# Kernel optimization log

Measured on AMD Instinct MI355X. Metric: run time of the kernel, lower is better.

## Reference

```python
import jax, jax.numpy as jnp
import numpy as np

D_MODEL = 1024
N_HEADS = 16
HEAD_DIM = D_MODEL // N_HEADS
B, S = 2, 2048


def setup_inputs() -> dict:
    key = jax.random.key(0)
    ks = jax.random.split(key, 10)
    lin = lambda k: jax.random.normal(k, (D_MODEL, D_MODEL), jnp.float32) / np.sqrt(D_MODEL)
    return {
        "x": jax.random.normal(ks[0], (B, S, D_MODEL), jnp.float32),
        "W_boundary": lin(ks[1]),
        "b_boundary": jax.random.normal(ks[2], (D_MODEL,), jnp.float32) * 0.02,
        "W_q": lin(ks[3]),
        "b_q": jax.random.normal(ks[4], (D_MODEL,), jnp.float32) * 0.02,
        "W_k": lin(ks[5]),
        "b_k": jax.random.normal(ks[6], (D_MODEL,), jnp.float32) * 0.02,
        "W_v": lin(ks[7]),
        "b_v": jax.random.normal(ks[8], (D_MODEL,), jnp.float32) * 0.02,
        "radial_weights": jax.random.normal(ks[9], (N_HEADS, 1, 1), jnp.float32),
        "tropical_scale": jnp.ones((1,), jnp.float32),
    }


def tropical_softmax(x, scale):
    # max-plus algebra softmax: subtract max, rescale, normalize with eps
    x = (x - jnp.max(x, axis=-1, keepdims=True)) * scale
    e = jnp.exp(x)
    return e / (jnp.sum(e, axis=-1, keepdims=True) + 1e-8)


def reference(x, W_boundary, b_boundary, W_q, b_q, W_k, b_k, W_v, b_v,
              radial_weights, tropical_scale):
    bsz, seq, _ = x.shape
    boundary = x @ W_boundary.T + b_boundary  # [B,S,D]

    def heads(W, b):  # [B,S,D] -> [B,H,S,hd]
        return (x @ W.T + b).reshape(bsz, seq, N_HEADS, HEAD_DIM).transpose(0, 2, 1, 3)

    q = heads(W_q, b_q)
    k = heads(W_k, b_k)
    v = heads(W_v, b_v)

    q = q * jax.nn.sigmoid(radial_weights)  # broadcast [H,1,1]

    scores = jnp.einsum("bhqd,bhkd->bhqk", q, k) / np.sqrt(HEAD_DIM).astype(np.float32)
    attn = tropical_softmax(scores, tropical_scale)  # [B,H,S,S]

    out = jnp.einsum("bhqk,bhkd->bhqd", attn, v)
    out = out.transpose(0, 2, 1, 3).reshape(bsz, seq, D_MODEL)
    out = out + boundary
    return (out, attn)
```

## Files before the change

### kernel.cpp

```cpp
#include <hip/hip_runtime.h>

#define DM 1024
#define NH 16
#define HD 64
#define BB 2
#define SS 2048
#define MTOT (BB*SS)
#define NTOT (4*DM)

typedef __attribute__((ext_vector_type(8))) short short8;
typedef __attribute__((ext_vector_type(4))) float f32x4;

#define MFMA(a,b,c) __builtin_amdgcn_mfma_f32_16x16x32_bf16((a),(b),(c),0,0,0)

__device__ inline unsigned short f2bf(float f) {
  union { float f; unsigned u; } v; v.f = f;
  unsigned r = v.u + 0x7FFFu + ((v.u >> 16) & 1u);
  return (unsigned short)(r >> 16);
}

__device__ inline void gload_lds16(const void* g, void* l) {
  void* gnc = const_cast<void*>(g);
  __builtin_amdgcn_global_load_lds(
      (__attribute__((address_space(1))) void*)gnc,
      (__attribute__((address_space(3))) void*)l, 16, 0, 0);
}

__global__ __launch_bounds__(256) void k_convert(
    const float* __restrict__ x, const float* __restrict__ w0,
    const float* __restrict__ w1, const float* __restrict__ w2,
    const float* __restrict__ w3,
    unsigned short* __restrict__ xb, unsigned short* __restrict__ wb) {
  const int T4 = (MTOT * DM) / 4;
  int stride = gridDim.x * blockDim.x;
  for (int i = blockIdx.x * blockDim.x + threadIdx.x; i < 2 * T4; i += stride) {
    const float* src; unsigned short* dst;
    if (i < T4) { src = x + (size_t)i * 4; dst = xb + (size_t)i * 4; }
    else {
      int flat = (i - T4) * 4;
      int sel = flat >> 20;
      int off = flat & ((1 << 20) - 1);
      const float* w = (sel == 0) ? w0 : (sel == 1) ? w1 : (sel == 2) ? w2 : w3;
      src = w + off; dst = wb + flat;
    }
    float4 v = *(const float4*)src;
    ushort4 o; o.x = f2bf(v.x); o.y = f2bf(v.y); o.z = f2bf(v.z); o.w = f2bf(v.w);
    *(ushort4*)dst = o;
  }
}

__global__ __launch_bounds__(256) void k_proj(
    const unsigned short* __restrict__ xb, const unsigned short* __restrict__ wb,
    const float* __restrict__ bbd, const float* __restrict__ bq,
    const float* __restrict__ bk, const float* __restrict__ bv,
    const float* __restrict__ radial,
    float* __restrict__ outbd,
    unsigned short* __restrict__ qb, unsigned short* __restrict__ kb,
    unsigned short* __restrict__ vb) {
  __shared__ unsigned short lsA[128 * 64];
  __shared__ unsigned short lsB[128 * 64];
  const int tid = threadIdx.x;
  const int wave = tid >> 6, lane = tid & 63;
  const int wr = wave >> 1, wc = wave & 1;
  const int lin = blockIdx.y * gridDim.x + blockIdx.x;
  const int swz = (lin & 7) * 128 + (lin >> 3);
  const int m0 = (swz >> 5) * 128, n0 = (swz & 31) * 128;
  const int ro = lane & 15, gg = lane >> 4;
  const int srow = lane >> 3;
  const int scol = (lane & 7) * 8;
  f32x4 acc[4][4] = {};
  for (int kt = 0; kt < DM / 64; ++kt) {
    __syncthreads();
    #pragma unroll
    for (int i = 0; i < 4; ++i) {
      int c = wave * 4 + i;
      const unsigned short* ga = xb + (size_t)(m0 + c * 8 + srow) * DM + kt * 64 + scol;
      gload_lds16(ga, (void*)(lsA + c * 512));
      const unsigned short* gb = wb + (size_t)(n0 + c * 8 + srow) * DM + kt * 64 + scol;
      gload_lds16(gb, (void*)(lsB + c * 512));
    }
    __syncthreads();
    #pragma unroll
    for (int ks = 0; ks < 2; ++ks) {
      short8 a[4], b[4];
      int ko = ks * 32 + gg * 8;
      #pragma unroll
      for (int r = 0; r < 4; ++r)
        a[r] = *(const short8*)&lsA[(wr * 64 + r * 16 + ro) * 64 + ko];
      #pragma unroll
      for (int c = 0; c < 4; ++c)
        b[c] = *(const short8*)&lsB[(wc * 64 + c * 16 + ro) * 64 + ko];
      #pragma unroll
      for (int r = 0; r < 4; ++r)
        #pragma unroll
        for (int c = 0; c < 4; ++c)
          acc[r][c] = MFMA(a[r], b[c], acc[r][c]);
    }
  }
  const int which = n0 >> 10;
  #pragma unroll
  for (int r = 0; r < 4; ++r) {
    const int mbase = m0 + wr * 64 + r * 16 + gg * 4;
    #pragma unroll
    for (int c = 0; c < 4; ++c) {
      const int n = n0 + wc * 64 + c * 16 + ro;
      const int nn = n & 1023;
      #pragma unroll
      for (int j = 0; j < 4; ++j) {
        const int m = mbase + j;
        float v = acc[r][c][j];
        if (which == 0) {
          outbd[(size_t)m * DM + nn] = v + bbd[nn];
        } else {
          const int h = nn >> 6, d = nn & 63;
          const int b2 = m >> 11, s = m & 2047;
          const size_t o = (((size_t)(b2 * NH + h)) * SS + s) * HD + d;
          if (which == 1) {
            float sg = 1.f / (1.f + __expf(-radial[h]));
            qb[o] = f2bf((v + bq[nn]) * sg);
          } else if (which == 2) {
            kb[o] = f2bf(v + bk[nn]);
          } else {
            vb[o] = f2bf(v + bv[nn]);
          }
        }
      }
    }
  }
}

__global__ __launch_bounds__(256) void k_vt(
    const unsigned short* __restrict__ vb, unsigned short* __restrict__ vt) {
  __shared__ unsigned short t[64][65];
  const int bh = blockIdx.y, st = blockIdx.x;
  const int tid = threadIdx.x;
  const int r = tid >> 2, c4 = (tid & 3) * 16;
  const unsigned short* src = vb + ((size_t)bh * SS + st * 64 + r) * HD + c4;
  #pragma unroll
  for (int i = 0; i < 16; i += 4) {
    ushort4 v = *(const ushort4*)(src + i);
    t[r][c4 + i + 0] = v.x; t[r][c4 + i + 1] = v.y;
    t[r][c4 + i + 2] = v.z; t[r][c4 + i + 3] = v.w;
  }
  __syncthreads();
  const int dd = tid >> 2, s4 = (tid & 3) * 16;
  unsigned short* dst = vt + ((size_t)bh * HD + dd) * SS + st * 64 + s4;
  #pragma unroll
  for (int i = 0; i < 16; i += 4) {
    ushort4 o;
    o.x = t[s4 + i + 0][dd]; o.y = t[s4 + i + 1][dd];
    o.z = t[s4 + i + 2][dd]; o.w = t[s4 + i + 3][dd];
    *(ushort4*)(dst + i) = o;
  }
}

__global__ __launch_bounds__(256) void k_attn_pv(
    const unsigned short* __restrict__ qb, const unsigned short* __restrict__ kb,
    const unsigned short* __restrict__ vt, const float* __restrict__ tsc,
    float* __restrict__ attn, float* __restrict__ out) {
  __shared__ unsigned short lk[2][64 * 64];
  __shared__ unsigned short lv[2][64 * 64];
  __shared__ __align__(16) unsigned short pt[4][16 * 64];
  const int bh = blockIdx.y, qt = blockIdx.x;
  const int tid = threadIdx.x, wave = tid >> 6, lane = tid & 63;
  const int ro = lane & 15, gg = lane >> 4;

  const unsigned short* kb_bh = kb + (size_t)bh * SS * HD;
  const unsigned short* vt_bh = vt + (size_t)bh * HD * SS;

  int sr0, sc0, sr1, sc1;
  {
    int s0 = (wave * 2 + 0) * 64 + lane;
    int s1 = (wave * 2 + 1) * 64 + lane;
    sr0 = s0 >> 3; sc0 = (s0 & 7) ^ (sr0 & 7);
    sr1 = s1 >> 3; sc1 = (s1 & 7) ^ (sr1 & 7);
  }

#define STAGE_K(buf, kt) do { \
    const unsigned short* g = kb_bh + (size_t)(kt) * 64 * HD; \
    gload_lds16(g + sr0 * 64 + sc0 * 8, (void*)(lk[buf] + (wave * 2 + 0) * 512)); \
    gload_lds16(g + sr1 * 64 + sc1 * 8, (void*)(lk[buf] + (wave * 2 + 1) * 512)); \
  } while (0)
#define STAGE_V(buf, kt) do { \
    const unsigned short* g = vt_bh + (size_t)(kt) * 64; \
    gload_lds16(g + (size_t)sr0 * SS + sc0 * 8, (void*)(lv[buf] + (wave * 2 + 0) * 512)); \
    gload_lds16(g + (size_t)sr1 * SS + sc1 * 8, (void*)(lv[buf] + (wave * 2 + 1) * 512)); \
  } while (0)

  STAGE_K(0, 0);

  const unsigned short* qrow =
      qb + ((size_t)bh * SS + qt * 64 + wave * 16 + ro) * HD;
  short8 aq0 = *(const short8*)(qrow + gg * 8);
  short8 aq1 = *(const short8*)(qrow + 32 + gg * 8);
  const float fac = tsc[0] * 0.125f;

  __syncthreads();

  float psum = 0.f;
  int cur = 0;
  for (int ct = 0; ct < 32; ++ct) {
    if (ct < 31) STAGE_K(cur ^ 1, ct + 1);
    const unsigned short* kbuf = lk[cur];
    #pragma unroll
    for (int sub = 0; sub < 4; ++sub) {
      const int rr = sub * 16 + ro;
      const unsigned short* kr = kbuf + rr * 64;
      short8 b0 = *(const short8*)&kr[(gg ^ (rr & 7)) * 8];
      short8 b1 = *(const short8*)&kr[((4 + gg) ^ (rr & 7)) * 8];
      f32x4 sf = {};
      sf = MFMA(b0, aq0, sf);
      sf = MFMA(b1, aq1, sf);
      psum += __expf(sf[0] * fac) + __expf(sf[1] * fac)
            + __expf(sf[2] * fac) + __expf(sf[3] * fac);
    }
    __syncthreads();
    cur ^= 1;
  }
  STAGE_K(0, 0);
  STAGE_V(0, 0);
  psum += __shfl_xor(psum, 16);
  psum += __shfl_xor(psum, 32);
  const float rsum = 1.f / (psum + 1e-8f);
  __syncthreads();

  float* ab = attn + ((size_t)bh * SS + qt * 64 + wave * 16 + ro) * SS;
  unsigned short* pw = &pt[wave][0];
  f32x4 acc[4] = {};
  cur = 0;
  for (int ct = 0; ct < 32; ++ct) {
    asm volatile("s_waitcnt vmcnt(4)" ::: "memory");
    __builtin_amdgcn_s_barrier();
    if (ct < 31) { STAGE_K(cur ^ 1, ct + 1); STAGE_V(cur ^ 1, ct + 1); }
    const unsigned short* kbuf = lk[cur];
    const unsigned short* vbuf = lv[cur];
    #pragma unroll
    for (int sub = 0; sub < 4; ++sub) {
      const int rr = sub * 16 + ro;
      const unsigned short* kr = kbuf + rr * 64;
      short8 b0 = *(const short8*)&kr[(gg ^ (rr & 7)) * 8];
      short8 b1 = *(const short8*)&kr[((4 + gg) ^ (rr & 7)) * 8];
      f32x4 sf = {};
      sf = MFMA(b0, aq0, sf);
      sf = MFMA(b1, aq1, sf);
      f32x4 st;
      st[0] = __expf(sf[0] * fac) * rsum; st[1] = __expf(sf[1] * fac) * rsum;
      st[2] = __expf(sf[2] * fac) * rsum; st[3] = __expf(sf[3] * fac) * rsum;
      __builtin_nontemporal_store(st, (f32x4*)(ab + (ct * 4 + sub) * 16 + gg * 4));
      unsigned w0, w1;
      asm("v_cvt_pk_bf16_f32 %0, %1, %2" : "=v"(w0) : "v"(st[0]), "v"(st[1]));
      asm("v_cvt_pk_bf16_f32 %0, %1, %2" : "=v"(w1) : "v"(st[2]), "v"(st[3]));
      const int slot = (sub * 2 + (gg >> 1)) ^ (ro & 7);
      *(uint2*)((char*)pw + ro * 128 + slot * 16 + (gg & 1) * 8) = make_uint2(w0, w1);
    }
    #pragma unroll
    for (int ks = 0; ks < 2; ++ks) {
      const int pslot = (ks * 4 + gg) ^ (ro & 7);
      short8 pa = *(const short8*)((const char*)pw + ro * 128 + pslot * 16);
      #pragma unroll
      for (int dc = 0; dc < 4; ++dc) {
        const int rr = dc * 16 + ro;
        const int cc = (ks * 4 + gg) ^ (rr & 7);
        short8 bvf = *(const short8*)&vbuf[rr * 64 + cc * 8];
        acc[dc] = MFMA(pa, bvf, acc[dc]);
      }
    }
    cur ^= 1;
  }

  const int b2 = bh >> 4, h = bh & 15;
  const int s0 = qt * 64 + wave * 16 + gg * 4;
  #pragma unroll
  for (int dc = 0; dc < 4; ++dc)
    #pragma unroll
    for (int j = 0; j < 4; ++j) {
      size_t o = ((size_t)b2 * SS + s0 + j) * DM + h * HD + dc * 16 + ro;
      out[o] += acc[dc][j];
    }
#undef STAGE_K
#undef STAGE_V
}

extern "C" void kernel_launch(void* const* d_in, const int* in_sizes, int n_in,
                              void* d_out, int out_size, void* d_ws, size_t ws_size,
                              hipStream_t stream) {
  (void)in_sizes; (void)n_in; (void)out_size; (void)ws_size;
  const float* x   = (const float*)d_in[0];
  const float* Wb  = (const float*)d_in[1];
  const float* bb  = (const float*)d_in[2];
  const float* Wq  = (const float*)d_in[3];
  const float* bq  = (const float*)d_in[4];
  const float* Wk  = (const float*)d_in[5];
  const float* bk  = (const float*)d_in[6];
  const float* Wv  = (const float*)d_in[7];
  const float* bv  = (const float*)d_in[8];
  const float* rad = (const float*)d_in[9];
  const float* tsc = (const float*)d_in[10];

  float* out  = (float*)d_out;
  float* attn = out + (size_t)MTOT * DM;

  unsigned short* qb = (unsigned short*)d_ws;
  unsigned short* kb = qb + (size_t)4 * 1024 * 1024;
  unsigned short* vt = kb + (size_t)4 * 1024 * 1024;

  unsigned short* xb = (unsigned short*)attn;
  unsigned short* wb = xb + (size_t)4 * 1024 * 1024;
  unsigned short* vb = wb + (size_t)4 * 1024 * 1024;

  k_convert<<<2048, 256, 0, stream>>>(x, Wb, Wq, Wk, Wv, xb, wb);
  k_proj<<<dim3(32, 32), 256, 0, stream>>>(xb, wb, bb, bq, bk, bv, rad, out, qb, kb, vb);
  k_vt<<<dim3(32, 32), 256, 0, stream>>>(vb, vt);
  k_attn_pv<<<dim3(32, 32), 256, 0, stream>>>(qb, kb, vt, tsc, attn, out);
}
```

Baseline: 276.8 us.

## Deepen K prefetch to 4-stage ring in pass 1 and swizzle block order

Pass 1 of the attention kernel now uses a 4-buffer LDS ring with three K tiles in flight, replacing the double buffer and full __syncthreads with vmcnt waits plus barriers. The LDS is unified into one array that pass 2 reuses as K/V double buffers. The block index is also remapped so consecutive blocks spread across heads, which is meant to improve L2 locality or XCD distribution. The aim is to hide global-load latency in the score-recompute pass, at the cost of tighter manual waitcnt bookkeeping.

```diff
diff --git a/kernel.cpp b/kernel.cpp
--- a/kernel.cpp
+++ b/kernel.cpp
@@ -158,10 +158,11 @@
     const unsigned short* __restrict__ qb, const unsigned short* __restrict__ kb,
     const unsigned short* __restrict__ vt, const float* __restrict__ tsc,
     float* __restrict__ attn, float* __restrict__ out) {
-  __shared__ unsigned short lk[2][64 * 64];
-  __shared__ unsigned short lv[2][64 * 64];
+  __shared__ unsigned short lds[4][64 * 64];
   __shared__ __align__(16) unsigned short pt[4][16 * 64];
-  const int bh = blockIdx.y, qt = blockIdx.x;
+  const int p = blockIdx.y * gridDim.x + blockIdx.x;
+  const int t = (p & 7) * 128 + (p >> 3);
+  const int bh = t >> 5, qt = t & 31;
   const int tid = threadIdx.x, wave = tid >> 6, lane = tid & 63;
   const int ro = lane & 15, gg = lane >> 4;
 
@@ -178,16 +179,14 @@
 
 #define STAGE_K(buf, kt) do { \
     const unsigned short* g = kb_bh + (size_t)(kt) * 64 * HD; \
-    gload_lds16(g + sr0 * 64 + sc0 * 8, (void*)(lk[buf] + (wave * 2 + 0) * 512)); \
-    gload_lds16(g + sr1 * 64 + sc1 * 8, (void*)(lk[buf] + (wave * 2 + 1) * 512)); \
+    gload_lds16(g + sr0 * 64 + sc0 * 8, (void*)(lds[buf] + (wave * 2 + 0) * 512)); \
+    gload_lds16(g + sr1 * 64 + sc1 * 8, (void*)(lds[buf] + (wave * 2 + 1) * 512)); \
   } while (0)
 #define STAGE_V(buf, kt) do { \
     const unsigned short* g = vt_bh + (size_t)(kt) * 64; \
-    gload_lds16(g + (size_t)sr0 * SS + sc0 * 8, (void*)(lv[buf] + (wave * 2 + 0) * 512)); \
-    gload_lds16(g + (size_t)sr1 * SS + sc1 * 8, (void*)(lv[buf] + (wave * 2 + 1) * 512)); \
+    gload_lds16(g + (size_t)sr0 * SS + sc0 * 8, (void*)(lds[buf] + (wave * 2 + 0) * 512)); \
+    gload_lds16(g + (size_t)sr1 * SS + sc1 * 8, (void*)(lds[buf] + (wave * 2 + 1) * 512)); \
   } while (0)
-
-  STAGE_K(0, 0);
 
   const unsigned short* qrow =
       qb + ((size_t)bh * SS + qt * 64 + wave * 16 + ro) * HD;
@@ -195,13 +194,11 @@
   short8 aq1 = *(const short8*)(qrow + 32 + gg * 8);
   const float fac = tsc[0] * 0.125f;
 
-  __syncthreads();
+  STAGE_K(0, 0); STAGE_K(1, 1); STAGE_K(2, 2);
 
   float psum = 0.f;
-  int cur = 0;
-  for (int ct = 0; ct < 32; ++ct) {
-    if (ct < 31) STAGE_K(cur ^ 1, ct + 1);
-    const unsigned short* kbuf = lk[cur];
+  auto p1body = [&](int ct) {
+    const unsigned short* kbuf = lds[ct & 3];
     #pragma unroll
     for (int sub = 0; sub < 4; ++sub) {
       const int rr = sub * 16 + ro;
@@ -214,26 +211,40 @@
       psum += __expf(sf[0] * fac) + __expf(sf[1] * fac)
             + __expf(sf[2] * fac) + __expf(sf[3] * fac);
     }
-    __syncthreads();
-    cur ^= 1;
-  }
+  };
+  for (int ct = 0; ct < 30; ++ct) {
+    asm volatile("s_waitcnt vmcnt(4)" ::: "memory");
+    __builtin_amdgcn_s_barrier();
+    if (ct < 29) STAGE_K((ct + 3) & 3, ct + 3);
+    p1body(ct);
+  }
+  asm volatile("s_waitcnt vmcnt(2)" ::: "memory");
+  __builtin_amdgcn_s_barrier();
+  p1body(30);
+  asm volatile("s_waitcnt vmcnt(0)" ::: "memory");
+  __builtin_amdgcn_s_barrier();
+  p1body(31);
+
   STAGE_K(0, 0);
-  STAGE_V(0, 0);
+  STAGE_V(1, 0);
   psum += __shfl_xor(psum, 16);
   psum += __shfl_xor(psum, 32);
   const float rsum = 1.f / (psum + 1e-8f);
-  __syncthreads();
+  asm volatile("s_waitcnt vmcnt(0)" ::: "memory");
+  __builtin_amdgcn_s_barrier();
 
   float* ab = attn + ((size_t)bh * SS + qt * 64 + wave * 16 + ro) * SS;
   unsigned short* pw = &pt[wave][0];
   f32x4 acc[4] = {};
-  cur = 0;
   for (int ct = 0; ct < 32; ++ct) {
     asm volatile("s_waitcnt vmcnt(4)" ::: "memory");
     __builtin_amdgcn_s_barrier();
-    if (ct < 31) { STAGE_K(cur ^ 1, ct + 1); STAGE_V(cur ^ 1, ct + 1); }
-    const unsigned short* kbuf = lk[cur];
-    const unsigned short* vbuf = lv[cur];
+    if (ct < 31) {
+      STAGE_K(2 * ((ct + 1) & 1), ct + 1);
+      STAGE_V(2 * ((ct + 1) & 1) + 1, ct + 1);
+    }
+    const unsigned short* kbuf = lds[2 * (ct & 1)];
+    const unsigned short* vbuf = lds[2 * (ct & 1) + 1];
     #pragma unroll
     for (int sub = 0; sub < 4; ++sub) {
       const int rr = sub * 16 + ro;
@@ -265,7 +276,6 @@
         acc[dc] = MFMA(pa, bvf, acc[dc]);
       }
     }
-    cur ^= 1;
   }
 
   const int b2 = bh >> 4, h = bh & 15;
```

Result: slower. 288.6 us (+4.2%).
